# Optimization experiments

Measured on AMD Instinct MI355X. Metric: run time of the kernel, lower is better.

## Reference

```python
import jax, jax.numpy as jnp
import numpy as np

B, T, C, H = 4, 1024, 768, 12
HD = C // H  # 64
EPS = 1e-5

def setup_inputs() -> dict:
    key = jax.random.key(0)
    ks = jax.random.split(key, 6)
    s = 0.02
    return {
        "x": jax.random.normal(ks[0], (B, T, C), jnp.float32),
        "ln1_w": jnp.ones((C,), jnp.float32),
        "w_attn": jax.random.normal(ks[1], (C, 3 * C), jnp.float32) * s,
        "w_pos": jax.random.normal(ks[2], (C, C), jnp.float32) * s,
        "w_cproj": jax.random.normal(ks[3], (C, C), jnp.float32) * s,
        "ln2_w": jnp.ones((C,), jnp.float32),
        "w_fc": jax.random.normal(ks[4], (C, 4 * C), jnp.float32) * s,
        "w_mproj": jax.random.normal(ks[5], (4 * C, C), jnp.float32) * s,
    }

def _layernorm(x, w):
    m = jnp.mean(x, axis=-1, keepdims=True)
    v = jnp.mean(jnp.square(x - m), axis=-1, keepdims=True)
    return (x - m) * jax.lax.rsqrt(v + EPS) * w

def _rpe_table(dtype):
    # sinusoidal table over relative distances [-(T-1), T-1] -> [2T-1, HD]
    inv_freq = 1.0 / (10000.0 ** (jnp.arange(0, HD, 2, dtype=jnp.float32) / HD))
    dist = jnp.arange(-(T - 1), T, dtype=jnp.float32)
    freqs = dist[:, None] * inv_freq[None, :]
    return jnp.concatenate([jnp.sin(freqs), jnp.cos(freqs)], axis=-1).astype(dtype)

def reference(x, ln1_w, w_attn, w_pos, w_cproj, ln2_w, w_fc, w_mproj):
    # ---- attention branch ----
    h = _layernorm(x, ln1_w)
    qkv = h @ w_attn                                 # [B,T,3C]
    q, k, v = jnp.split(qkv, 3, axis=-1)
    q = q.reshape(B, T, H, HD).transpose(0, 2, 1, 3)  # [B,H,T,HD]
    k = k.reshape(B, T, H, HD).transpose(0, 2, 1, 3)
    v = v.reshape(B, T, H, HD).transpose(0, 2, 1, 3)
    # note: the original also computes p = c_pos(x) but never uses it (dead code)

    # relative position embeddings gathered to [T,T,HD]
    idx = jnp.arange(T)
    rel = jnp.clip(idx[:, None] - idx[None, :], -(T - 1), T - 1) + (T - 1)
    rpe = _rpe_table(q.dtype)[rel]                    # [T,T,HD]

    scale = 1.0 / np.sqrt(HD)
    att = (jnp.einsum('bhid,bhjd->bhij', q, k)
           + jnp.einsum('bhid,ijd->bhij', q, rpe)) * scale
    causal = idx[:, None] >= idx[None, :]             # [T,T] lower-tri
    att = jnp.where(causal, att, -jnp.inf)
    att = jax.nn.softmax(att, axis=-1)
    y = jnp.einsum('bhij,bhjd->bhid', att, v)         # [B,H,T,HD]
    y = y.transpose(0, 2, 1, 3).reshape(B, T, C) @ w_cproj
    x = x + y

    # ---- MLP branch ----
    h2 = _layernorm(x, ln2_w)
    m = jax.nn.gelu(h2 @ w_fc, approximate=False) @ w_mproj
    return x + m
```

## Files before the change

kernel.cpp:

```cpp
#include <hip/hip_runtime.h>
#include <math.h>

typedef __attribute__((ext_vector_type(8))) short bf16x8;
typedef __attribute__((ext_vector_type(4))) float f32x4;
typedef __attribute__((ext_vector_type(16))) float f32x16;
typedef __attribute__((ext_vector_type(4))) unsigned u32x4;

__device__ inline short f2bf(float f) {
  unsigned u = __builtin_bit_cast(unsigned, f);
  u = u + 0x7fffu + ((u >> 16) & 1u);
  return (short)(u >> 16);
}
__device__ inline float bf2f(short s) {
  return __builtin_bit_cast(float, ((unsigned)(unsigned short)s) << 16);
}
__device__ inline unsigned cvt_pk_bf16(float lo, float hi) {
  unsigned r;
  asm("v_cvt_pk_bf16_f32 %0, %1, %2" : "=v"(r) : "v"(lo), "v"(hi));
  return r;
}

__device__ inline void gload16(const short* g, const short* l) {
  __builtin_amdgcn_global_load_lds(
      (const __attribute__((address_space(1))) unsigned*)g,
      (__attribute__((address_space(3))) unsigned*)(short*)l, 16, 0, 0);
}

__global__ __launch_bounds__(256) void wtrans_all(
    const float* __restrict__ wa, const float* __restrict__ wc,
    const float* __restrict__ wf, const float* __restrict__ wm,
    short* __restrict__ oa, short* __restrict__ oc,
    short* __restrict__ of, short* __restrict__ om) {
  __shared__ float tile[32][33];
  int blk = blockIdx.x;
  const float* in; short* out; int K, N, bx;
  if (blk < 1728)      { in = wa; out = oa; K = 768;  N = 2304; bx = 72; }
  else if (blk < 2304) { blk -= 1728; in = wc; out = oc; K = 768;  N = 768;  bx = 24; }
  else if (blk < 4608) { blk -= 2304; in = wf; out = of; K = 768;  N = 3072; bx = 96; }
  else                 { blk -= 4608; in = wm; out = om; K = 3072; N = 768;  bx = 24; }
  const int n0 = (blk % bx) * 32, k0 = (blk / bx) * 32;
  const int tx = threadIdx.x & 31, ty = threadIdx.x >> 5;
  #pragma unroll
  for (int r = ty; r < 32; r += 8)
    tile[r][tx] = in[(size_t)(k0 + r) * N + n0 + tx];
  __syncthreads();
  #pragma unroll
  for (int r = ty; r < 32; r += 8)
    out[(size_t)(n0 + r) * K + k0 + tx] = f2bf(tile[tx][r]);
}

__global__ __launch_bounds__(256) void qv_kernel(
    const short* __restrict__ qkv, short* __restrict__ qpr,
    short* __restrict__ ktab, short* __restrict__ vT) {
  __shared__ short tile[64][65];
  if (blockIdx.x < 6144) {
    const int idx = blockIdx.x * 256 + threadIdx.x;
    const int cc = idx & 31;
    const int row = idx >> 5;
    const int i = row & 1023, bh = row >> 10;
    const int b = bh / 12, h = bh % 12;
    const float invf = exp2f(-(float)cc * (13.287712379549449f / 32.0f));
    const float ang = (float)i * invf;
    float si, co;
    __sincosf(ang, &si, &co);
    if (bh == 0) {
      ktab[i * 64 + cc]      = f2bf(co);
      ktab[i * 64 + 32 + cc] = f2bf(si);
    }
    const short* q = qkv + (size_t)(b * 1024 + i) * 2304 + h * 64;
    const float qs = bf2f(q[cc]), qc = bf2f(q[32 + cc]);
    qpr[(size_t)row * 64 + cc]      = f2bf(qs * si + qc * co);
    qpr[(size_t)row * 64 + 32 + cc] = f2bf(qc * si - qs * co);
  } else {
    const int blk = blockIdx.x - 6144;
    const int bh = blk >> 4, t0 = (blk & 15) * 64;
    const int b = bh / 12, h = bh % 12;
    const int tx = threadIdx.x & 63, ty = threadIdx.x >> 6;
    const short* src = qkv + (size_t)(b * 1024 + t0) * 2304 + 1536 + h * 64;
    #pragma unroll
    for (int r = ty; r < 64; r += 4)
      tile[r][tx] = src[(size_t)r * 2304 + tx];
    __syncthreads();
    short* dst = vT + (size_t)bh * 64 * 1024 + t0;
    #pragma unroll
    for (int r = ty; r < 64; r += 4)
      dst[(size_t)r * 1024 + tx] = tile[tx][r];
  }
}

__global__ __launch_bounds__(256) void ln_kernel(
    const float* __restrict__ x, const float* __restrict__ w,
    short* __restrict__ out) {
  const int row = blockIdx.x, tid = threadIdx.x;
  const float* xr = x + (size_t)row * 768;
  float v0 = xr[tid], v1 = xr[tid + 256], v2 = xr[tid + 512];
  float s = v0 + v1 + v2;
  #pragma unroll
  for (int o = 1; o < 64; o <<= 1) s += __shfl_xor(s, o);
  __shared__ float red[8];
  const int wv = tid >> 6;
  if ((tid & 63) == 0) red[wv] = s;
  __syncthreads();
  const float mean = (red[0] + red[1] + red[2] + red[3]) * (1.0f / 768.0f);
  v0 -= mean; v1 -= mean; v2 -= mean;
  float q = v0 * v0 + v1 * v1 + v2 * v2;
  #pragma unroll
  for (int o = 1; o < 64; o <<= 1) q += __shfl_xor(q, o);
  if ((tid & 63) == 0) red[4 + wv] = q;
  __syncthreads();
  const float var = (red[4] + red[5] + red[6] + red[7]) * (1.0f / 768.0f);
  const float inv = 1.0f / sqrtf(var + 1e-5f);
  out[(size_t)row * 768 + tid]       = f2bf(v0 * inv * w[tid]);
  out[(size_t)row * 768 + tid + 256] = f2bf(v1 * inv * w[tid + 256]);
  out[(size_t)row * 768 + tid + 512] = f2bf(v2 * inv * w[tid + 512]);
}

template <int EPI, int BM, int BN>
__global__ __launch_bounds__(256) void gemm3u(
    const short* __restrict__ A, const short* __restrict__ Bt,
    const float* __restrict__ res, float* __restrict__ outF,
    short* __restrict__ outB, int M, int N, int K, int lda, int ldb) {
  __shared__ __align__(16) short As[3][BM * 32];
  __shared__ __align__(16) short Bs[3][BN * 32];
  constexpr int WM = BM / 2, WN = BN / 2;
  constexpr int MI = WM / 16, NJ = WN / 16;
  constexpr int NA = BM / 64, NB = BN / 64;
  constexpr int G = NA + NB;
  const int tid = threadIdx.x;
  const int w = tid >> 6, lane = tid & 63;
  const int gx = gridDim.x, gy = gridDim.y;
  const int nwg = gx * gy * gridDim.z;
  const int lin = blockIdx.x + gx * (blockIdx.y + gy * blockIdx.z);
  const int wg = (lin & 7) * (nwg >> 3) + (lin >> 3);
  const int bxi = wg % gx;
  const int tmp = wg / gx;
  const int byi = tmp % gy, bzi = tmp / gy;
  const int m0 = byi * BM, n0 = bxi * BN;
  const int wm = (w >> 1) * WM, wn = (w & 1) * WN;
  const int lr = lane >> 2;
  const int lc = (lane & 3) * 8;
  if constexpr (EPI == 3) {
    A += (size_t)bzi * K;
    Bt += (size_t)bzi * K;
    outF += (size_t)bzi * (size_t)M * N;
  }
  f32x4 acc[MI][NJ];
  #pragma unroll
  for (int i = 0; i < MI; i++)
    #pragma unroll
    for (int j = 0; j < NJ; j++)
      #pragma unroll
      for (int r = 0; r < 4; r++) acc[i][j][r] = 0.0f;

  const int nt = K / 32;
  const short* pA[NA];
  const short* pB[NB];
  #pragma unroll
  for (int p = 0; p < NA; ++p)
    pA[p] = A + (size_t)(m0 + p * 64 + w * 16 + lr) * lda + lc;
  #pragma unroll
  for (int p = 0; p < NB; ++p)
    pB[p] = Bt + (size_t)(n0 + p * 64 + w * 16 + lr) * ldb + lc;
  const int aoff = (wm + (lane & 15)) * 32 + (lane >> 4) * 8;
  const int boff = (wn + (lane & 15)) * 32 + (lane >> 4) * 8;

#define STAGE(SB)                                                              \
  do {                                                                         \
    _Pragma("unroll") for (int p = 0; p < NA; ++p) {                           \
      gload16(pA[p], &As[SB][p * 2048 + w * 512]);                             \
      pA[p] += 32;                                                             \
    }                                                                          \
    _Pragma("unroll") for (int p = 0; p < NB; ++p) {                           \
      gload16(pB[p], &Bs[SB][p * 2048 + w * 512]);                             \
      pB[p] += 32;                                                             \
    }                                                                          \
  } while (0)

#define STEP(CB, SB, DOSTAGE, LAST)                                            \
  do {                                                                         \
    if (LAST) asm volatile("s_waitcnt vmcnt(0)" ::: "memory");                 \
    else      asm volatile("s_waitcnt vmcnt(%0)" :: "n"(G) : "memory");        \
    __builtin_amdgcn_s_barrier();                                              \
    __builtin_amdgcn_sched_barrier(0);                                         \
    bf16x8 af[MI], bfr[NJ];                                                    \
    _Pragma("unroll") for (int i = 0; i < MI; i++)                             \
      af[i] = *(const bf16x8*)&As[CB][aoff + i * 512];                         \
    _Pragma("unroll") for (int j = 0; j < NJ; j++)                             \
      bfr[j] = *(const bf16x8*)&Bs[CB][boff + j * 512];                        \
    if (DOSTAGE) STAGE(SB);                                                    \
    _Pragma("unroll") for (int i = 0; i < MI; i++)                             \
      _Pragma("unroll") for (int j = 0; j < NJ; j++)                           \
        acc[i][j] = __builtin_amdgcn_mfma_f32_16x16x32_bf16(                   \
            af[i], bfr[j], acc[i][j], 0, 0, 0);                                \
  } while (0)

  STAGE(0);
  STAGE(1);
  const int ntri = nt / 3;
  for (int ti = 0; ti < ntri - 1; ++ti) {
    STEP(0, 2, 1, 0);
    STEP(1, 0, 1, 0);
    STEP(2, 1, 1, 0);
  }
  STEP(0, 2, 1, 0);
  STEP(1, 0, 0, 0);
  STEP(2, 0, 0, 1);
#undef STEP
#undef STAGE

  const int r0 = (lane >> 4) * 4, cl = lane & 15;
  #pragma unroll
  for (int i = 0; i < MI; i++) {
    #pragma unroll
    for (int j = 0; j < NJ; j++) {
      const int gm = m0 + wm + i * 16 + r0;
      const int gn = n0 + wn + j * 16 + cl;
      #pragma unroll
      for (int r = 0; r < 4; r++) {
        const size_t idx = (size_t)(gm + r) * N + gn;
        const float v = acc[i][j][r];
        if constexpr (EPI == 0) {
          outB[idx] = f2bf(v);
        } else if constexpr (EPI == 1) {
          outF[idx] = res[idx] + v;
        } else if constexpr (EPI == 2) {
          outB[idx] = f2bf(0.5f * v * (1.0f + erff(v * 0.70710678118f)));
        } else {
          outF[idx] = v;
        }
      }
    }
  }
}

__global__ __launch_bounds__(256) void reduce_splitk(
    const float* __restrict__ Cp, const float* __restrict__ res,
    float* __restrict__ out) {
  const size_t i4 = ((size_t)blockIdx.x * 256 + threadIdx.x) * 4;
  float4 a = *(const float4*)(res + i4);
  #pragma unroll
  for (int z = 0; z < 2; ++z) {
    float4 p = *(const float4*)(Cp + (size_t)z * 3145728 + i4);
    a.x += p.x; a.y += p.y; a.z += p.z; a.w += p.w;
  }
  *(float4*)(out + i4) = a;
}

__global__ __launch_bounds__(512) void attn_part8(
    const short* __restrict__ qkv, const short* __restrict__ vT,
    const short* __restrict__ qpr, const short* __restrict__ ktab,
    float* __restrict__ mpart, float* __restrict__ lpart,
    short* __restrict__ Ypart) {
  __shared__ __align__(16) short Ka[2][32 * 136];
  __shared__ __align__(16) short Va[2][64 * 40];
  const int bx = blockIdx.x;
  const int bh = bx / 20;
  const int r = bx % 20;
  int c, sub;
  if (r < 4)        { c = 0; sub = r; }
  else if (r < 8)   { c = 1; sub = r - 4; }
  else if (r < 11)  { c = 2; sub = r - 8; }
  else if (r < 14)  { c = 3; sub = r - 11; }
  else if (r < 16)  { c = 4; sub = r - 14; }
  else if (r < 18)  { c = 5; sub = r - 16; }
  else if (r == 18) { c = 6; sub = 0; }
  else              { c = 7; sub = 0; }
  const int tid = threadIdx.x;
  const int w = tid >> 6;
  const int lane = tid & 63;
  const int li = lane & 31, hi = lane >> 5;
  const int it = 4 * c + sub * 8 + w;
  const bool valid = (it <= 31);
  const int b = bh / 12, h = bh % 12;
  const int I0 = (valid ? it : 31) * 32;
  const int jt0 = 4 * c;
  const int jtmax = valid ? ((it < jt0 + 3) ? it : jt0 + 3) : (jt0 - 1);
  constexpr float SCALE2 = 0.125f * 1.44269504089f;

  const short* kbase = qkv + (size_t)(b * 1024) * 2304 + 768 + h * 64;
  const short* vbase = vT + (size_t)bh * 64 * 1024;

  const int krow = tid >> 4, kch = tid & 15;
  const short* ksrc = (kch < 8) ? (kbase + kch * 8) : (ktab + (kch - 8) * 8);
  const size_t kstr = (kch < 8) ? 2304 : 64;
  const int vrow = tid >> 2, vch = tid & 3;

  int4 kreg, vreg;
  {
    const int J0 = jt0 * 32;
    kreg = *(const int4*)(ksrc + (size_t)(J0 + krow) * kstr);
    if (tid < 256)
      vreg = *(const int4*)(vbase + (size_t)vrow * 1024 + J0 + vch * 8);
  }

  const short* qrow = qkv + (size_t)(b * 1024 + I0 + li) * 2304 + h * 64;
  const short* qprow = qpr + ((size_t)bh * 1024 + I0 + li) * 64;
  bf16x8 qf[8];
  #pragma unroll
  for (int s = 0; s < 4; s++) {
    qf[s]     = *(const bf16x8*)(qrow + s * 16 + hi * 8);
    qf[4 + s] = *(const bf16x8*)(qprow + s * 16 + hi * 8);
  }

  *(int4*)&Ka[0][krow * 136 + kch * 8] = kreg;
  if (tid < 256) *(int4*)&Va[0][vrow * 40 + vch * 8] = vreg;
  __syncthreads();

  float m_run = -1e30f, l_run = 0.0f;
  f32x16 ya0, ya1;
  #pragma unroll
  for (int q = 0; q < 16; q++) { ya0[q] = 0.0f; ya1[q] = 0.0f; }

  for (int t = 0; t < 4; ++t) {
    const int cur = t & 1;
    if (t < 3) {
      const int J0n = (jt0 + t + 1) * 32;
      kreg = *(const int4*)(ksrc + (size_t)(J0n + krow) * kstr);
      if (tid < 256)
        vreg = *(const int4*)(vbase + (size_t)vrow * 1024 + J0n + vch * 8);
    }
    const int jt = jt0 + t;
    if (jt <= jtmax) {
      bf16x8 kf[8];
      #pragma unroll
      for (int s = 0; s < 8; s++)
        kf[s] = *(const bf16x8*)&Ka[cur][li * 136 + s * 16 + hi * 8];
      bf16x8 vc[4];
      #pragma unroll
      for (int s = 0; s < 2; s++) {
        vc[s * 2]     = *(const bf16x8*)&Va[cur][li * 40 + s * 16 + hi * 8];
        vc[s * 2 + 1] = *(const bf16x8*)&Va[cur][(32 + li) * 40 + s * 16 + hi * 8];
      }
      f32x16 sa0, sa1;
      #pragma unroll
      for (int q = 0; q < 16; q++) { sa0[q] = 0.0f; sa1[q] = 0.0f; }
      __builtin_amdgcn_s_setprio(1);
      #pragma unroll
      for (int s = 0; s < 4; s++) {
        sa0 = __builtin_amdgcn_mfma_f32_32x32x16_bf16(kf[2 * s],     qf[2 * s],     sa0, 0, 0, 0);
        sa1 = __builtin_amdgcn_mfma_f32_32x32x16_bf16(kf[2 * s + 1], qf[2 * s + 1], sa1, 0, 0, 0);
      }
      __builtin_amdgcn_s_setprio(0);
      float sv[16];
      float mx = -1e30f;
      if (jt == it) {
        #pragma unroll
        for (int q = 0; q < 16; q++) {
          const int j = (q & 3) + 8 * (q >> 2) + 4 * hi;
          float v = (sa0[q] + sa1[q]) * SCALE2;
          v = (j <= li) ? v : -1e30f;
          sv[q] = v;
          mx = fmaxf(mx, v);
        }
      } else {
        #pragma unroll
        for (int q = 0; q < 16; q++) {
          const float v = (sa0[q] + sa1[q]) * SCALE2;
          sv[q] = v;
          mx = fmaxf(mx, v);
        }
      }
      mx = fmaxf(mx, __shfl_xor(mx, 32));
      float mref = m_run;
      float alpha = 1.0f;
      const bool resc = !__all(mx <= m_run + 11.5f);
      if (resc) {
        mref = fmaxf(m_run, mx);
        alpha = exp2f(m_run - mref);
        m_run = mref;
      }
      float psum = 0.0f;
      unsigned pw[8];
      #pragma unroll
      for (int q = 0; q < 8; q++) {
        const float p0 = exp2f(sv[2 * q] - mref);
        const float p1 = exp2f(sv[2 * q + 1] - mref);
        psum += p0 + p1;
        pw[q] = cvt_pk_bf16(p0, p1);
      }
      psum += __shfl_xor(psum, 32);
      l_run = l_run * alpha + psum;
      if (resc) {
        #pragma unroll
        for (int q = 0; q < 16; q++) {
          const int row = (q & 3) + 8 * (q >> 2) + 4 * hi;
          const float a = __shfl(alpha, row);
          ya0[q] *= a;
          ya1[q] *= a;
        }
      }
      #pragma unroll
      for (int s = 0; s < 2; s++) {
        unsigned a0 = pw[4 * s],     b0 = pw[4 * s + 2];
        unsigned a1 = pw[4 * s + 1], b1 = pw[4 * s + 3];
        asm volatile("v_permlane32_swap_b32 %0, %1" : "+v"(a0), "+v"(b0));
        asm volatile("v_permlane32_swap_b32 %0, %1" : "+v"(a1), "+v"(b1));
        u32x4 t4;
        t4[0] = a0; t4[1] = a1; t4[2] = b0; t4[3] = b1;
        const bf16x8 pf = __builtin_bit_cast(bf16x8, t4);
        __builtin_amdgcn_s_setprio(1);
        ya0 = __builtin_amdgcn_mfma_f32_32x32x16_bf16(pf, vc[s * 2],     ya0, 0, 0, 0);
        ya1 = __builtin_amdgcn_mfma_f32_32x32x16_bf16(pf, vc[s * 2 + 1], ya1, 0, 0, 0);
        __builtin_amdgcn_s_setprio(0);
      }
    }
    if (t < 3) {
      *(int4*)&Ka[cur ^ 1][krow * 136 + kch * 8] = kreg;
      if (tid < 256) *(int4*)&Va[cur ^ 1][vrow * 40 + vch * 8] = vreg;
    }
    __syncthreads();
  }
  if (!valid) return;
  const int task = bh * 144 + it + 30 * c - 2 * c * c;
  if (hi == 0) {
    mpart[(size_t)task * 32 + li] = m_run;
    lpart[(size_t)task * 32 + li] = l_run;
  }
  short* yb = Ypart + (size_t)task * 2048;
  #pragma unroll
  for (int q = 0; q < 16; q++) {
    const int row = (q & 3) + 8 * (q >> 2) + 4 * hi;
    yb[row * 64 + li]      = f2bf(ya0[q]);
    yb[row * 64 + 32 + li] = f2bf(ya1[q]);
  }
}

__global__ __launch_bounds__(256) void attn_combine(
    const float* __restrict__ mpart, const float* __restrict__ lpart,
    const short* __restrict__ Ypart, short* __restrict__ yout) {
  const int blk = blockIdx.x;
  const int it = blk & 31, bh = blk >> 5;
  const int b = bh / 12, h = bh % 12;
  const int g = it >> 2;
  const int nc = g + 1;
  const int row = threadIdx.x >> 3;
  const int c0 = (threadIdx.x & 7) * 8;
  float mv[8], lv[8], wgt[8];
  float m = -1e30f;
  #pragma unroll
  for (int cI = 0; cI < 8; ++cI) {
    const int idx = bh * 144 + it + 30 * cI - 2 * cI * cI;
    mv[cI] = (cI < nc) ? mpart[(size_t)idx * 32 + row] : -1e30f;
    lv[cI] = (cI < nc) ? lpart[(size_t)idx * 32 + row] : 0.0f;
    m = fmaxf(m, mv[cI]);
  }
  float L = 0.0f;
  #pragma unroll
  for (int cI = 0; cI < 8; ++cI) {
    wgt[cI] = exp2f(mv[cI] - m);
    L += lv[cI] * wgt[cI];
  }
  const float inv = 1.0f / L;
  float y[8];
  #pragma unroll
  for (int r = 0; r < 8; r++) y[r] = 0.0f;
  #pragma unroll
  for (int cI = 0; cI < 8; ++cI) {
    if (cI < nc) {
      const int idx = bh * 144 + it + 30 * cI - 2 * cI * cI;
      bf16x8 v = *(const bf16x8*)(Ypart + ((size_t)idx * 32 + row) * 64 + c0);
      #pragma unroll
      for (int r = 0; r < 8; r++) y[r] += bf2f(v[r]) * wgt[cI];
    }
  }
  short* dst = yout + (size_t)(b * 1024 + it * 32 + row) * 768 + h * 64 + c0;
  #pragma unroll
  for (int r = 0; r < 8; r++) dst[r] = f2bf(y[r] * inv);
}

extern "C" void kernel_launch(void* const* d_in, const int* in_sizes, int n_in,
                              void* d_out, int out_size, void* d_ws, size_t ws_size,
                              hipStream_t stream) {
  const float* x       = (const float*)d_in[0];
  const float* ln1_w   = (const float*)d_in[1];
  const float* w_attn  = (const float*)d_in[2];
  const float* w_cproj = (const float*)d_in[4];
  const float* ln2_w   = (const float*)d_in[5];
  const float* w_fc    = (const float*)d_in[6];
  const float* w_mproj = (const float*)d_in[7];
  float* out = (float*)d_out;
  char* ws = (char*)d_ws;

  short* wT_attn  = (short*)(ws + 0);
  short* wT_cproj = (short*)(ws + 3538944);
  short* wT_fc    = (short*)(ws + 4718592);
  short* wT_mproj = (short*)(ws + 9437184);
  short* ktab     = (short*)(ws + 14155776);
  short* h_bf     = (short*)(ws + 14417920);
  short* qpr      = (short*)(ws + 14417920);
  short* qkv_bf   = (short*)(ws + 20709376);
  short* vT       = (short*)(ws + 39583744);
  short* y_att    = (short*)(ws + 45875200);
  short* h2_bf    = (short*)(ws + 52166656);
  short* hfc_bf   = (short*)(ws + 58458112);
  float* mpart = (float*)(ws + 52166656);
  float* lpart = (float*)(ws + 53051392);
  short* Ypart = (short*)(ws + 53936128);
  float* Cpart = (float*)(ws + 20709376);

  wtrans_all<<<6912, 256, 0, stream>>>(w_attn, w_cproj, w_fc, w_mproj,
                                       wT_attn, wT_cproj, wT_fc, wT_mproj);

  ln_kernel<<<4096, 256, 0, stream>>>(x, ln1_w, h_bf);
  gemm3u<0, 128, 128><<<dim3(18, 32), 256, 0, stream>>>(
      h_bf, wT_attn, nullptr, nullptr, qkv_bf, 4096, 2304, 768, 768, 768);
  qv_kernel<<<6912, 256, 0, stream>>>(qkv_bf, qpr, ktab, vT);
  attn_part8<<<960, 512, 0, stream>>>(qkv_bf, vT, qpr, ktab, mpart, lpart, Ypart);
  attn_combine<<<1536, 256, 0, stream>>>(mpart, lpart, Ypart, y_att);
  gemm3u<1, 64, 64><<<dim3(12, 64), 256, 0, stream>>>(
      y_att, wT_cproj, x, out, nullptr, 4096, 768, 768, 768, 768);
  ln_kernel<<<4096, 256, 0, stream>>>(out, ln2_w, h2_bf);
  gemm3u<2, 128, 128><<<dim3(24, 32), 256, 0, stream>>>(
      h2_bf, wT_fc, nullptr, nullptr, hfc_bf, 4096, 3072, 768, 768, 768);
  gemm3u<3, 128, 64><<<dim3(12, 32, 2), 256, 0, stream>>>(
      hfc_bf, wT_mproj, nullptr, Cpart, nullptr, 4096, 768, 1536, 3072, 3072);
  reduce_splitk<<<3072, 256, 0, stream>>>(Cpart, out, out);
}
```

Before: 192.7 us.

## Add per-wave private-LDS GEMM for QKV, FC and MLP-proj with 3-way split-K

```diff
diff --git a/kernel.cpp b/kernel.cpp
--- a/kernel.cpp
+++ b/kernel.cpp
@@ -115,6 +115,116 @@
   out[(size_t)row * 768 + tid + 512] = f2bf(v2 * inv * w[tid + 512]);
 }
 
+template <int EPI>
+__global__ __launch_bounds__(256) void gemmW(
+    const short* __restrict__ A, const short* __restrict__ Bt,
+    float* __restrict__ outF, short* __restrict__ outB,
+    int M, int N, int K, int lda, int ldb) {
+  __shared__ __align__(16) short lds[4 * 2 * 2 * 2048];
+  const int tid = threadIdx.x;
+  const int w = tid >> 6, lane = tid & 63;
+  const int gx = gridDim.x, gy = gridDim.y;
+  const int nwg = gx * gy * gridDim.z;
+  const int lin = blockIdx.x + gx * (blockIdx.y + gy * blockIdx.z);
+  const int wg = (lin & 7) * (nwg >> 3) + (lin >> 3);
+  const int bxi = wg % gx;
+  const int tmp = wg / gx;
+  const int byi = tmp % gy, bzi = tmp / gy;
+  if constexpr (EPI == 3) {
+    A += (size_t)bzi * K;
+    Bt += (size_t)bzi * K;
+    outF += (size_t)bzi * (size_t)M * N;
+  }
+  const int wm = byi * 128 + (w >> 1) * 64;
+  const int wn = bxi * 128 + (w & 1) * 64;
+  const int lr = lane >> 2;
+  const int sc = ((lane & 3) ^ ((lane >> 3) & 3)) * 8;
+  const short* pA[4];
+  const short* pB[4];
+  #pragma unroll
+  for (int p = 0; p < 4; ++p) {
+    pA[p] = A + (size_t)(wm + p * 16 + lr) * lda + sc;
+    pB[p] = Bt + (size_t)(wn + p * 16 + lr) * ldb + sc;
+  }
+  const int fr = lane & 15, c4 = lane >> 4;
+  const int foff = fr * 32 + (c4 ^ ((fr >> 1) & 3)) * 8;
+  short* const base = &lds[w * 8192];
+
+  f32x4 acc[4][4];
+  #pragma unroll
+  for (int i = 0; i < 4; i++)
+    #pragma unroll
+    for (int j = 0; j < 4; j++)
+      #pragma unroll
+      for (int r = 0; r < 4; r++) acc[i][j][r] = 0.0f;
+
+  const int nt = K / 32;
+
+#define WSTAGE(S)                                                              \
+  do {                                                                         \
+    short* d = base + (S) * 4096;                                              \
+    _Pragma("unroll") for (int p = 0; p < 4; ++p) {                            \
+      gload16(pA[p], d + p * 512);                                             \
+      pA[p] += 32;                                                             \
+    }                                                                          \
+    _Pragma("unroll") for (int p = 0; p < 4; ++p) {                            \
+      gload16(pB[p], d + 2048 + p * 512);                                      \
+      pB[p] += 32;                                                             \
+    }                                                                          \
+  } while (0)
+
+  WSTAGE(0);
+  WSTAGE(1);
+  for (int t = 0; t < nt; ++t) {
+    if (t + 1 < nt)
+      asm volatile("s_waitcnt vmcnt(8)" ::: "memory");
+    else
+      asm volatile("s_waitcnt vmcnt(0)" ::: "memory");
+    __builtin_amdgcn_sched_barrier(0);
+    const int cb = t & 1;
+    const short* s = base + cb * 4096;
+    bf16x8 af[4], bfr[4];
+    #pragma unroll
+    for (int i = 0; i < 4; i++)
+      af[i] = *(const bf16x8*)&s[foff + i * 512];
+    #pragma unroll
+    for (int j = 0; j < 4; j++)
+      bfr[j] = *(const bf16x8*)&s[2048 + foff + j * 512];
+    asm volatile("s_waitcnt lgkmcnt(0)" ::: "memory");
+    __builtin_amdgcn_sched_barrier(0);
+    if (t + 2 < nt) WSTAGE(cb);
+    #pragma unroll
+    for (int i = 0; i < 4; i++)
+      #pragma unroll
+      for (int j = 0; j < 4; j++)
+        acc[i][j] = __builtin_amdgcn_mfma_f32_16x16x32_bf16(af[i], bfr[j],
+                                                            acc[i][j], 0, 0, 0);
+  }
+#undef WSTAGE
+
+  const int r0 = (lane >> 4) * 4, cl = lane & 15;
+  #pragma unroll
+  for (int i = 0; i < 4; i++) {
+    #pragma unroll
+    for (int j = 0; j < 4; j++) {
+      const int gm = wm + i * 16 + r0;
+      const int gn = wn + j * 16 + cl;
+      #pragma unroll
+      for (int r = 0; r < 4; r++) {
+        const size_t idx = (size_t)(gm + r) * N + gn;
+        const float v = acc[i][j][r];
+        if constexpr (EPI == 0) {
+          outB[idx] = f2bf(v);
+        } else if constexpr (EPI == 2) {
+          outB[idx] = f2bf(0.5f * v * (1.0f + erff(v * 0.70710678118f)));
+        } else {
+          outF[idx] = v;
+        }
+      }
+    }
+  }
+}
+
 template <int EPI, int BM, int BN>
 __global__ __launch_bounds__(256) void gemm3u(
     const short* __restrict__ A, const short* __restrict__ Bt,
@@ -134,16 +244,11 @@
   const int wg = (lin & 7) * (nwg >> 3) + (lin >> 3);
   const int bxi = wg % gx;
   const int tmp = wg / gx;
-  const int byi = tmp % gy, bzi = tmp / gy;
+  const int byi = tmp % gy;
   const int m0 = byi * BM, n0 = bxi * BN;
   const int wm = (w >> 1) * WM, wn = (w & 1) * WN;
   const int lr = lane >> 2;
   const int lc = (lane & 3) * 8;
-  if constexpr (EPI == 3) {
-    A += (size_t)bzi * K;
-    Bt += (size_t)bzi * K;
-    outF += (size_t)bzi * (size_t)M * N;
-  }
   f32x4 acc[MI][NJ];
   #pragma unroll
   for (int i = 0; i < MI; i++)
@@ -219,14 +324,10 @@
       for (int r = 0; r < 4; r++) {
         const size_t idx = (size_t)(gm + r) * N + gn;
         const float v = acc[i][j][r];
-        if constexpr (EPI == 0) {
+        if constexpr (EPI == 1) {
+          outF[idx] = res[idx] + v;
+        } else {
           outB[idx] = f2bf(v);
-        } else if constexpr (EPI == 1) {
-          outF[idx] = res[idx] + v;
-        } else if constexpr (EPI == 2) {
-          outB[idx] = f2bf(0.5f * v * (1.0f + erff(v * 0.70710678118f)));
-        } else {
-          outF[idx] = v;
         }
       }
     }
@@ -239,7 +340,7 @@
   const size_t i4 = ((size_t)blockIdx.x * 256 + threadIdx.x) * 4;
   float4 a = *(const float4*)(res + i4);
   #pragma unroll
-  for (int z = 0; z < 2; ++z) {
+  for (int z = 0; z < 3; ++z) {
     float4 p = *(const float4*)(Cp + (size_t)z * 3145728 + i4);
     a.x += p.x; a.y += p.y; a.z += p.z; a.w += p.w;
   }
@@ -502,17 +603,17 @@
                                        wT_attn, wT_cproj, wT_fc, wT_mproj);
 
   ln_kernel<<<4096, 256, 0, stream>>>(x, ln1_w, h_bf);
-  gemm3u<0, 128, 128><<<dim3(18, 32), 256, 0, stream>>>(
-      h_bf, wT_attn, nullptr, nullptr, qkv_bf, 4096, 2304, 768, 768, 768);
+  gemmW<0><<<dim3(18, 32), 256, 0, stream>>>(
+      h_bf, wT_attn, nullptr, qkv_bf, 4096, 2304, 768, 768, 768);
   qv_kernel<<<6912, 256, 0, stream>>>(qkv_bf, qpr, ktab, vT);
   attn_part8<<<960, 512, 0, stream>>>(qkv_bf, vT, qpr, ktab, mpart, lpart, Ypart);
   attn_combine<<<1536, 256, 0, stream>>>(mpart, lpart, Ypart, y_att);
   gemm3u<1, 64, 64><<<dim3(12, 64), 256, 0, stream>>>(
       y_att, wT_cproj, x, out, nullptr, 4096, 768, 768, 768, 768);
   ln_kernel<<<4096, 256, 0, stream>>>(out, ln2_w, h2_bf);
-  gemm3u<2, 128, 128><<<dim3(24, 32), 256, 0, stream>>>(
-      h2_bf, wT_fc, nullptr, nullptr, hfc_bf, 4096, 3072, 768, 768, 768);
-  gemm3u<3, 128, 64><<<dim3(12, 32, 2), 256, 0, stream>>>(
-      hfc_bf, wT_mproj, nullptr, Cpart, nullptr, 4096, 768, 1536, 3072, 3072);
+  gemmW<2><<<dim3(24, 32), 256, 0, stream>>>(
+      h2_bf, wT_fc, nullptr, hfc_bf, 4096, 3072, 768, 768, 768);
+  gemmW<3><<<dim3(6, 32, 3), 256, 0, stream>>>(
+      hfc_bf, wT_mproj, Cpart, nullptr, 4096, 768, 1024, 3072, 3072);
   reduce_splitk<<<3072, 256, 0, stream>>>(Cpart, out, out);
 }
```

Measured after the change: 220.6 us. 1.14x slower.
